# Kernel optimization log

Measured on AMD Instinct MI355X. Metric: run time of the kernel, lower is better.

The kernel has to match this reference:

```python
import jax, jax.numpy as jnp
import numpy as np

KH, KW = 3, 3
STRIDE = (1, 1)


def setup_inputs() -> dict:
    key = jax.random.key(0)
    k1, k2, k3 = jax.random.split(key, 3)
    N, C, H, W = 16, 128, 64, 64
    O = 128
    x = jax.random.normal(k1, (N, C, H, W), dtype=jnp.float32)
    # Flat weight layout [O, C*KH*KW], matching torch reshape of [O,C,KH,KW]
    weight = jax.random.normal(k2, (O, C * KH * KW), dtype=jnp.float32) * 0.02
    bias = jax.random.normal(k3, (O, 1), dtype=jnp.float32) * 0.02
    return {"x": x, "weight": weight, "bias": bias}


def reference(x, weight, bias):
    O = weight.shape[0]
    C = x.shape[1]
    # [O, C*KH*KW] -> [O, C, KH, KW]; flattening order (C major, then kh, kw)
    # matches the module's unfold/permute im2col layout.
    w4 = weight.reshape(O, C, KH, KW)
    out = jax.lax.conv_general_dilated(
        x, w4,
        window_strides=STRIDE,
        padding='VALID',
        dimension_numbers=('NCHW', 'OIHW', 'NCHW'),
    )
    return out + bias.reshape(1, O, 1, 1)
```

## Files before the change

kernel.cpp:

```cpp
#include <hip/hip_runtime.h>
#include <stdint.h>

#define AS_G __attribute__((address_space(1)))
#define AS_L __attribute__((address_space(3)))

typedef __bf16 bf16x8 __attribute__((ext_vector_type(8)));
typedef float  f32x4  __attribute__((ext_vector_type(4)));

static constexpr int NIMG = 16, CIN = 128, H = 64, W = 64, OCH = 128;
static constexpr int HO = 62, WO = 62;
static constexpr int PIX = HO * WO;
static constexpr int M_TOT = NIMG * PIX;
static constexpr int K_TOT = CIN * 9;
static constexpr int BM = 64, BK = 64;
static constexpr int KSTEPS = K_TOT / BK;
static constexpr int NWG = M_TOT / BM;

__device__ __forceinline__ unsigned short f2bf(float f) {
    union { float f; uint32_t u; } v; v.f = f;
    uint32_t u = v.u;
    return (unsigned short)((u + 0x7FFFu + ((u >> 16) & 1u)) >> 16);
}

__global__ __launch_bounds__(256) void prep_kernel(const float* __restrict__ x,
                                                   const float* __restrict__ wsrc,
                                                   unsigned short* __restrict__ xt,
                                                   unsigned short* __restrict__ bpd) {
    __shared__ float lds[CIN][W + 4];
    if (blockIdx.x < NIMG * H) {
        const int n   = blockIdx.x >> 6;
        const int h   = blockIdx.x & 63;
        const int tid = threadIdx.x;
        {
            const int c  = tid >> 1;
            const int w0 = (tid & 1) * 32;
            const float* src = x + (((size_t)(n * CIN + c) * H + h) * W + w0);
            #pragma unroll
            for (int j = 0; j < 8; ++j) {
                float4 v = *reinterpret_cast<const float4*>(src + j * 4);
                *reinterpret_cast<float4*>(&lds[c][w0 + j * 4]) = v;
            }
        }
        __syncthreads();
        {
            const int w  = tid >> 2;
            const int c0 = (tid & 3) * 32;
            unsigned short* dst = xt + (((size_t)(n * H + h) * W + w) * CIN + c0);
            uint32_t pk[16];
            #pragma unroll
            for (int j = 0; j < 16; ++j) {
                uint32_t lo = f2bf(lds[c0 + 2 * j][w]);
                uint32_t hi = f2bf(lds[c0 + 2 * j + 1][w]);
                pk[j] = lo | (hi << 16);
            }
            #pragma unroll
            for (int j = 0; j < 4; ++j) {
                *reinterpret_cast<uint4*>(dst + j * 8) =
                    make_uint4(pk[4 * j], pk[4 * j + 1], pk[4 * j + 2], pk[4 * j + 3]);
            }
        }
    } else {
        int tid = (blockIdx.x - NIMG * H) * 256 + threadIdx.x;
        if (tid < OCH * K_TOT) {
            int o  = tid / K_TOT;
            int kp = tid - o * K_TOT;
            int t  = kp >> 7;
            int c  = kp & 127;
            bpd[tid] = f2bf(wsrc[o * K_TOT + c * 9 + t]);
        }
    }
}

__global__ __launch_bounds__(256) void gemm_kernel(const unsigned short* __restrict__ xt,
                                                   const unsigned short* __restrict__ bp,
                                                   const float* __restrict__ bias,
                                                   float* __restrict__ out) {
    __shared__ alignas(16) unsigned short As[BM * BK];
    __shared__ alignas(16) unsigned short Bs[OCH * BK];
    const int tid  = threadIdx.x;
    const int wv   = tid >> 6;
    const int lane = tid & 63;

    const int orig = blockIdx.x;
    const int xcd  = orig & 7;
    const int idx  = orig >> 3;
    const int wg   = (xcd == 0 ? 0 : 121 + (xcd - 1) * 120) + idx;
    const int m0   = wg * BM;

    const int csel = ((lane & 7) ^ (lane >> 3)) * 8;
    int aBase[2], bBase[4];
    #pragma unroll
    for (int i = 0; i < 2; ++i) {
        int row = (wv * 2 + i) * 8 + (lane >> 3);
        int m = m0 + row;
        int n  = m / PIX;
        int r  = m - n * PIX;
        int y  = r / WO;
        int xx = r - y * WO;
        aBase[i] = ((n * H + y) * W + xx) * CIN;
    }
    #pragma unroll
    for (int i = 0; i < 4; ++i)
        bBase[i] = ((wv * 4 + i) * 8 + (lane >> 3)) * K_TOT;

    const int wr = wv >> 1, wc = wv & 1;
    const int lr = lane & 15, lq = lane >> 4;
    const int aRow = (wr * 32 + lr) * 128;
    const int bRow = (wc * 64 + lr) * 128;
    int colx[2];
    #pragma unroll
    for (int ks = 0; ks < 2; ++ks)
        colx[ks] = (ks * 64 + lq * 16) ^ ((lane & 7) << 4);

    f32x4 acc[2][4];
    #pragma unroll
    for (int a = 0; a < 2; ++a)
        #pragma unroll
        for (int b = 0; b < 4; ++b)
            acc[a][b] = (f32x4){0.f, 0.f, 0.f, 0.f};

    const char* AsB = (const char*)As;
    const char* BsB = (const char*)Bs;

    for (int step = 0; step < KSTEPS; ++step) {
        const int t  = step >> 1;
        const int c0 = (step & 1) * 64;
        const int tapoff = (t / 3) * (W * CIN) + (t % 3) * CIN + c0;
        const int kb = step * BK;
        #pragma unroll
        for (int i = 0; i < 2; ++i)
            __builtin_amdgcn_global_load_lds(
                (AS_G unsigned int*)(xt + aBase[i] + tapoff + csel),
                (AS_L unsigned int*)((char*)As + (wv * 2 + i) * 1024),
                16, 0, 0);
        #pragma unroll
        for (int i = 0; i < 4; ++i)
            __builtin_amdgcn_global_load_lds(
                (AS_G unsigned int*)(bp + bBase[i] + kb + csel),
                (AS_L unsigned int*)((char*)Bs + (wv * 4 + i) * 1024),
                16, 0, 0);
        __syncthreads();
        #pragma unroll
        for (int ks = 0; ks < 2; ++ks) {
            bf16x8 af[2], bfr[4];
            #pragma unroll
            for (int mi = 0; mi < 2; ++mi)
                af[mi] = *(const bf16x8*)(AsB + aRow + mi * 2048 + colx[ks]);
            #pragma unroll
            for (int ni = 0; ni < 4; ++ni)
                bfr[ni] = *(const bf16x8*)(BsB + bRow + ni * 2048 + colx[ks]);
            #pragma unroll
            for (int mi = 0; mi < 2; ++mi)
                #pragma unroll
                for (int ni = 0; ni < 4; ++ni)
                    acc[mi][ni] = __builtin_amdgcn_mfma_f32_16x16x32_bf16(
                        bfr[ni], af[mi], acc[mi][ni], 0, 0, 0);
        }
        __syncthreads();
    }

    f32x4 bv[4];
    #pragma unroll
    for (int ni = 0; ni < 4; ++ni)
        bv[ni] = *(const f32x4*)(bias + wc * 64 + ni * 16 + lq * 4);
    #pragma unroll
    for (int mi = 0; mi < 2; ++mi) {
        int m = m0 + wr * 32 + mi * 16 + lr;
        int n  = m / PIX;
        int r  = m - n * PIX;
        int y  = r / WO;
        int xx = r - y * WO;
        float* ob = out + (size_t)n * OCH * PIX + y * WO + xx;
        #pragma unroll
        for (int ni = 0; ni < 4; ++ni)
            #pragma unroll
            for (int j = 0; j < 4; ++j) {
                int o = wc * 64 + ni * 16 + lq * 4 + j;
                ob[(size_t)o * PIX] = acc[mi][ni][j] + bv[ni][j];
            }
    }
}

extern "C" void kernel_launch(void* const* d_in, const int* in_sizes, int n_in,
                              void* d_out, int out_size, void* d_ws, size_t ws_size,
                              hipStream_t stream) {
    const float* x    = (const float*)d_in[0];
    const float* wsrc = (const float*)d_in[1];
    const float* bias = (const float*)d_in[2];
    float* out = (float*)d_out;
    unsigned short* xt = (unsigned short*)d_ws;
    unsigned short* bp = xt + (size_t)NIMG * H * W * CIN;
    prep_kernel<<<dim3(NIMG * H + (OCH * K_TOT + 255) / 256), dim3(256), 0, stream>>>(
        x, wsrc, xt, bp);
    gemm_kernel<<<dim3(NWG), dim3(256), 0, stream>>>(xt, bp, bias, out);
}
```

Baseline: 43.53 us.

## Triple-buffer LDS staging in GEMM to overlap global loads with MFMA

Replaces the single-buffer load-sync-compute loop with a three-slot LDS ring: tile step t+2 is issued asynchronously while tile t is computed, and explicit vmcnt waits plus barriers let later loads stay in flight. It also raises wave priority around the MFMA block with s_setprio. The aim is to hide global-load latency that was exposed every K step. In exchange LDS use per workgroup grows (72 KB dynamic), which may reduce occupancy, and correctness now depends on the hand-set waitcnt values.

Measured after the change: 44.29 us. About the same (+1.7%).

```diff
diff --git a/kernel.cpp b/kernel.cpp
--- a/kernel.cpp
+++ b/kernel.cpp
@@ -15,6 +15,8 @@
 static constexpr int BM = 64, BK = 64;
 static constexpr int KSTEPS = K_TOT / BK;
 static constexpr int NWG = M_TOT / BM;
+static constexpr int SLOT = 24576;
+static constexpr int LDS_BYTES = 3 * SLOT;
 
 __device__ __forceinline__ unsigned short f2bf(float f) {
     union { float f; uint32_t u; } v; v.f = f;
@@ -75,8 +77,7 @@
                                                    const unsigned short* __restrict__ bp,
                                                    const float* __restrict__ bias,
                                                    float* __restrict__ out) {
-    __shared__ alignas(16) unsigned short As[BM * BK];
-    __shared__ alignas(16) unsigned short Bs[OCH * BK];
+    extern __shared__ char lds[];
     const int tid  = threadIdx.x;
     const int wv   = tid >> 6;
     const int lane = tid & 63;
@@ -103,6 +104,23 @@
     for (int i = 0; i < 4; ++i)
         bBase[i] = ((wv * 4 + i) * 8 + (lane >> 3)) * K_TOT;
 
+    auto stage = [&](char* dst, int step) {
+        const int t  = step >> 1;
+        const int c0 = (step & 1) * 64;
+        const int tapoff = (t / 3) * (W * CIN) + (t % 3) * CIN + c0;
+        const int kb = step * BK;
+        #pragma unroll
+        for (int i = 0; i < 2; ++i)
+            __builtin_amdgcn_global_load_lds(
+                (AS_G unsigned int*)(xt + aBase[i] + tapoff + csel),
+                (AS_L unsigned int*)(dst + (wv * 2 + i) * 1024), 16, 0, 0);
+        #pragma unroll
+        for (int i = 0; i < 4; ++i)
+            __builtin_amdgcn_global_load_lds(
+                (AS_G unsigned int*)(bp + bBase[i] + kb + csel),
+                (AS_L unsigned int*)(dst + 8192 + (wv * 4 + i) * 1024), 16, 0, 0);
+    };
+
     const int wr = wv >> 1, wc = wv & 1;
     const int lr = lane & 15, lq = lane >> 4;
     const int aRow = (wr * 32 + lr) * 128;
@@ -119,45 +137,51 @@
         for (int b = 0; b < 4; ++b)
             acc[a][b] = (f32x4){0.f, 0.f, 0.f, 0.f};
 
-    const char* AsB = (const char*)As;
-    const char* BsB = (const char*)Bs;
-
-    for (int step = 0; step < KSTEPS; ++step) {
-        const int t  = step >> 1;
-        const int c0 = (step & 1) * 64;
-        const int tapoff = (t / 3) * (W * CIN) + (t % 3) * CIN + c0;
-        const int kb = step * BK;
-        #pragma unroll
-        for (int i = 0; i < 2; ++i)
-            __builtin_amdgcn_global_load_lds(
-                (AS_G unsigned int*)(xt + aBase[i] + tapoff + csel),
-                (AS_L unsigned int*)((char*)As + (wv * 2 + i) * 1024),
-                16, 0, 0);
-        #pragma unroll
-        for (int i = 0; i < 4; ++i)
-            __builtin_amdgcn_global_load_lds(
-                (AS_G unsigned int*)(bp + bBase[i] + kb + csel),
-                (AS_L unsigned int*)((char*)Bs + (wv * 4 + i) * 1024),
-                16, 0, 0);
-        __syncthreads();
+    auto compute = [&](const char* base) {
         #pragma unroll
         for (int ks = 0; ks < 2; ++ks) {
             bf16x8 af[2], bfr[4];
             #pragma unroll
             for (int mi = 0; mi < 2; ++mi)
-                af[mi] = *(const bf16x8*)(AsB + aRow + mi * 2048 + colx[ks]);
+                af[mi] = *(const bf16x8*)(base + aRow + mi * 2048 + colx[ks]);
             #pragma unroll
             for (int ni = 0; ni < 4; ++ni)
-                bfr[ni] = *(const bf16x8*)(BsB + bRow + ni * 2048 + colx[ks]);
+                bfr[ni] = *(const bf16x8*)(base + 8192 + bRow + ni * 2048 + colx[ks]);
+            __builtin_amdgcn_s_setprio(1);
             #pragma unroll
             for (int mi = 0; mi < 2; ++mi)
                 #pragma unroll
                 for (int ni = 0; ni < 4; ++ni)
                     acc[mi][ni] = __builtin_amdgcn_mfma_f32_16x16x32_bf16(
                         bfr[ni], af[mi], acc[mi][ni], 0, 0, 0);
-        }
-        __syncthreads();
-    }
+            __builtin_amdgcn_s_setprio(0);
+        }
+    };
+
+    char* b0 = lds;
+    char* b1 = lds + SLOT;
+    char* b2 = lds + 2 * SLOT;
+    stage(b0, 0);
+    stage(b1, 1);
+    for (int t = 0; t < KSTEPS - 2; ++t) {
+        stage(b2, t + 2);
+        asm volatile("s_waitcnt vmcnt(12)" ::: "memory");
+        __builtin_amdgcn_s_barrier();
+        __builtin_amdgcn_sched_barrier(0);
+        compute(b0);
+        asm volatile("s_waitcnt lgkmcnt(0)" ::: "memory");
+        __builtin_amdgcn_s_barrier();
+        __builtin_amdgcn_sched_barrier(0);
+        char* tmp = b0; b0 = b1; b1 = b2; b2 = tmp;
+    }
+    asm volatile("s_waitcnt vmcnt(6)" ::: "memory");
+    __builtin_amdgcn_s_barrier();
+    __builtin_amdgcn_sched_barrier(0);
+    compute(b0);
+    asm volatile("s_waitcnt vmcnt(0)" ::: "memory");
+    __builtin_amdgcn_s_barrier();
+    __builtin_amdgcn_sched_barrier(0);
+    compute(b1);
 
     f32x4 bv[4];
     #pragma unroll
@@ -192,5 +216,5 @@
     unsigned short* bp = xt + (size_t)NIMG * H * W * CIN;
     prep_kernel<<<dim3(NIMG * H + (OCH * K_TOT + 255) / 256), dim3(256), 0, stream>>>(
         x, wsrc, xt, bp);
-    gemm_kernel<<<dim3(NWG), dim3(256), 0, stream>>>(xt, bp, bias, out);
-}
+    gemm_kernel<<<dim3(NWG), dim3(256), LDS_BYTES, stream>>>(xt, bp, bias, out);
+}
```
